# Optimization experiments

Hardware: AMD Instinct MI355X
Metric: run time of the kernel (lower is better)

The kernel has to match this reference:

```python
import jax, jax.numpy as jnp
import numpy as np

H = 128      # hidden_size
B = 8192     # number of sessions
L = 50       # items per session (constant here; code supports ragged)
T = B * L    # total tokens


def setup_inputs() -> dict:
    key = jax.random.key(0)
    ks = jax.random.split(key, 10)
    s = 1.0 / np.sqrt(H)
    u = lambda k, shape: jax.random.uniform(k, shape, jnp.float32, -s, s)
    return {
        "intra_item_emb": jax.random.normal(ks[0], (T, H), jnp.float32),
        "inter_item_emb": jax.random.normal(ks[1], (T, H), jnp.float32),
        "W1": u(ks[2], (H, H)), "b1": u(ks[3], (H,)),
        "W2": u(ks[4], (H, H)), "b2": u(ks[5], (H,)),
        "q_w": u(ks[6], (1, H)), "q_b": u(ks[7], (1,)),
        "W3": u(ks[8], (H, 2 * H)), "b3": u(ks[9], (H,)),
        "seq_len": jnp.full((B,), L, dtype=jnp.int32),
    }


def reference(intra_item_emb, inter_item_emb, W1, b1, W2, b2, q_w, q_b, W3, b3, seq_len):
    # max_fusing: elementwise max of the two embedding streams  [T, H]
    hidden = jnp.maximum(intra_item_emb, inter_item_emb)
    nB = seq_len.shape[0]
    nT = hidden.shape[0]
    # segment id per token and index of last token of each session
    seg_ids = jnp.repeat(jnp.arange(nB), seq_len, total_repeat_length=nT)  # [T]
    last_idx = jnp.cumsum(seq_len) - 1                                      # [B]
    v_n = hidden[last_idx]                 # [B, H] last node of each session
    v_n_rep = v_n[seg_ids]                 # [T, H] broadcast last node to tokens
    # attention weight per token: q(sigmoid(W1 v_n + W2 h))  [T, 1]
    alpha = jax.nn.sigmoid(v_n_rep @ W1.T + b1 + hidden @ W2.T + b2) @ q_w.T + q_b
    # segment-sum pooling of alpha-weighted tokens  [B, H]
    s_g = jax.ops.segment_sum(alpha * hidden, seg_ids, num_segments=nB)
    # final session representation  [B, H]
    h_s = jnp.concatenate([v_n, s_g], axis=1) @ W3.T + b3
    return h_s
```

## Files before the change

### kernel.cpp

```cpp
#include <hip/hip_runtime.h>
#include <hip/hip_bf16.h>

#define HDIM 128
#define RS 136

typedef __attribute__((ext_vector_type(8))) short short8;
typedef __attribute__((ext_vector_type(4))) float floatv4;

static __device__ __forceinline__ unsigned short f2bf(float f) {
  union { float f; unsigned u; } x; x.f = f;
  unsigned r = x.u + 0x7fffu + ((x.u >> 16) & 1u);
  return (unsigned short)(r >> 16);
}
static __device__ __forceinline__ float blo(unsigned u) { return __uint_as_float(u << 16); }
static __device__ __forceinline__ float bhi(unsigned u) { return __uint_as_float(u & 0xffff0000u); }

static __device__ __forceinline__ void sync_lds() {
  asm volatile("s_waitcnt lgkmcnt(0)" ::: "memory");
  __builtin_amdgcn_s_barrier();
  asm volatile("" ::: "memory");
}

__global__ void prep_kernel(const int* __restrict__ seq, int* __restrict__ offs, int B,
                            const float* __restrict__ W1, const float* __restrict__ W2,
                            const float* __restrict__ W3,
                            unsigned short* __restrict__ w1b, unsigned short* __restrict__ w2b,
                            unsigned short* __restrict__ w3b) {
  if (blockIdx.x == 0) {
    __shared__ int part[256];
    int tid = threadIdx.x;
    int chunk = (B + 255) >> 8;
    int beg = tid * chunk, end = min(beg + chunk, B);
    int s = 0;
    for (int i = beg; i < end; ++i) s += seq[i];
    part[tid] = s;
    __syncthreads();
    for (int d = 1; d < 256; d <<= 1) {
      int v = (tid >= d) ? part[tid - d] : 0;
      __syncthreads();
      part[tid] += v;
      __syncthreads();
    }
    int run = (tid == 0) ? 0 : part[tid - 1];
    for (int i = beg; i < end; ++i) { offs[i] = run; run += seq[i]; }
  } else {
    int i = (blockIdx.x - 1) * 256 + threadIdx.x;
    if (i < 16384) { w1b[i] = f2bf(W1[i]); w2b[i] = f2bf(W2[i]); }
    if (i < 32768) { w3b[i] = f2bf(W3[i]); }
  }
}

__global__ __launch_bounds__(256, 3) void session_kernel(
    const float* __restrict__ intra, const float* __restrict__ inter,
    const unsigned short* __restrict__ w1b, const float* __restrict__ b1,
    const unsigned short* __restrict__ w2b, const float* __restrict__ b2,
    const float* __restrict__ qw, const float* __restrict__ qb,
    const unsigned short* __restrict__ w3b, const float* __restrict__ b3,
    const int* __restrict__ seq, const int* __restrict__ offs,
    float* __restrict__ out, int B) {
  __shared__ unsigned short hbf[64 * RS];
  __shared__ unsigned short vnb[HDIM];
  __shared__ unsigned short sgb[HDIM];
  __shared__ float alphaAcc[64];
  __shared__ float sgpart[4][HDIM];

  const int tid = threadIdx.x;
  const int lane = tid & 63, wid = tid >> 6;
  const int quad = lane >> 4, lcol = lane & 15;
  const int nbase = wid << 5;
  const int n0 = nbase + lcol, n1 = n0 + 16;
  const int G = gridDim.x;

  const float qb0 = qb[0];
  const float bb0 = b1[n0] + b2[n0], bb1 = b1[n1] + b2[n1];
  const float q0 = qw[n0], q1 = qw[n1];
  const float b30 = b3[n0], b31 = b3[n1];

  short8 w2f[2][4];
  #pragma unroll
  for (int nt = 0; nt < 2; ++nt) {
    int nn = nbase + (nt << 4) + lcol;
    #pragma unroll
    for (int kt = 0; kt < 4; ++kt)
      w2f[nt][kt] = *(const short8*)(w2b + nn * HDIM + (kt << 5) + (quad << 3));
  }

  float4 ra[8], rb[8];
  int n_cur;
  {
    int s0 = blockIdx.x;
    n_cur = seq[s0]; if (n_cur > 64) n_cur = 64;
    int st0 = offs[s0];
    const float4* pa = (const float4*)(intra + (size_t)st0 * HDIM);
    const float4* pb = (const float4*)(inter + (size_t)st0 * HDIM);
    #pragma unroll
    for (int it = 0; it < 8; ++it) {
      int idx = (it << 8) + tid, t = idx >> 5;
      float4 z; z.x = 0.f; z.y = 0.f; z.z = 0.f; z.w = 0.f;
      float4 va = z, vb = z;
      if (t < n_cur) { va = pa[idx]; vb = pb[idx]; }
      ra[it] = va; rb[it] = vb;
    }
  }

  for (int s = blockIdx.x; s < B; s += G) {
    const int sn = s + G;
    int n_nxt = 0, st_nxt = 0;
    if (sn < B) { n_nxt = seq[sn]; if (n_nxt > 64) n_nxt = 64; st_nxt = offs[sn]; }

    const int lastrow = (n_cur > 0) ? (n_cur - 1) : 0;
    #pragma unroll
    for (int it = 0; it < 8; ++it) {
      int idx = (it << 8) + tid;
      int t = idx >> 5, j4 = idx & 31;
      float4 a = ra[it], c = rb[it];
      union { __hip_bfloat162 b; unsigned u; } p01, p23;
      p01.b = __float22bfloat162_rn(make_float2(fmaxf(a.x, c.x), fmaxf(a.y, c.y)));
      p23.b = __float22bfloat162_rn(make_float2(fmaxf(a.z, c.z), fmaxf(a.w, c.w)));
      uint2 st; st.x = p01.u; st.y = p23.u;
      *(uint2*)&hbf[t * RS + (j4 << 2)] = st;
      if (t == lastrow) *(uint2*)&vnb[j4 << 2] = st;
    }
    if (tid < 64) alphaAcc[tid] = qb0;
    sync_lds();

    float c0, c1;
    {
      floatv4 p0 = {0.f, 0.f, 0.f, 0.f}, p1 = {0.f, 0.f, 0.f, 0.f};
      #pragma unroll
      for (int kt = 0; kt < 4; ++kt) {
        short8 af = *(const short8*)&vnb[(kt << 5) + (quad << 3)];
        short8 bf0 = *(const short8*)(w1b + n0 * HDIM + (kt << 5) + (quad << 3));
        short8 bf1 = *(const short8*)(w1b + n1 * HDIM + (kt << 5) + (quad << 3));
        p0 = __builtin_amdgcn_mfma_f32_16x16x32_bf16(af, bf0, p0, 0, 0, 0);
        p1 = __builtin_amdgcn_mfma_f32_16x16x32_bf16(af, bf1, p1, 0, 0, 0);
      }
      c0 = p0[0] + bb0;
      c1 = p1[0] + bb1;
    }

    if (sn < B) {
      const float4* pa = (const float4*)(intra + (size_t)st_nxt * HDIM);
      const float4* pb = (const float4*)(inter + (size_t)st_nxt * HDIM);
      #pragma unroll
      for (int it = 0; it < 8; ++it) {
        int idx = (it << 8) + tid, t = idx >> 5;
        float4 z; z.x = 0.f; z.y = 0.f; z.z = 0.f; z.w = 0.f;
        float4 va = z, vb = z;
        if (t < n_nxt) { va = pa[idx]; vb = pb[idx]; }
        ra[it] = va; rb[it] = vb;
      }
    }
    asm volatile("" ::: "memory");

    #pragma unroll
    for (int mt = 0; mt < 4; ++mt) {
      floatv4 a0 = {c0, c0, c0, c0}, a1 = {c1, c1, c1, c1};
      const unsigned short* arow = &hbf[((mt << 4) + lcol) * RS + (quad << 3)];
      #pragma unroll
      for (int kt = 0; kt < 4; ++kt) {
        short8 af = *(const short8*)(arow + (kt << 5));
        a0 = __builtin_amdgcn_mfma_f32_16x16x32_bf16(af, w2f[0][kt], a0, 0, 0, 0);
        a1 = __builtin_amdgcn_mfma_f32_16x16x32_bf16(af, w2f[1][kt], a1, 0, 0, 0);
      }
      #pragma unroll
      for (int r = 0; r < 4; ++r) {
        float v = q0 * __builtin_amdgcn_rcpf(1.f + __expf(-a0[r]))
                + q1 * __builtin_amdgcn_rcpf(1.f + __expf(-a1[r]));
        v += __shfl_xor(v, 1, 64);
        v += __shfl_xor(v, 2, 64);
        v += __shfl_xor(v, 4, 64);
        v += __shfl_xor(v, 8, 64);
        if (lcol == 0) atomicAdd(&alphaAcc[(mt << 4) + (quad << 2) + r], v);
      }
    }
    sync_lds();

    {
      int jg = tid & 15, ts = tid >> 4;
      float ac[8];
      #pragma unroll
      for (int e = 0; e < 8; ++e) ac[e] = 0.f;
      #pragma unroll
      for (int tt = 0; tt < 4; ++tt) {
        int t = (tt << 4) + ts;
        float al = alphaAcc[t];
        uint4 u = *(const uint4*)&hbf[t * RS + (jg << 3)];
        ac[0] += al * blo(u.x); ac[1] += al * bhi(u.x);
        ac[2] += al * blo(u.y); ac[3] += al * bhi(u.y);
        ac[4] += al * blo(u.z); ac[5] += al * bhi(u.z);
        ac[6] += al * blo(u.w); ac[7] += al * bhi(u.w);
      }
      #pragma unroll
      for (int e = 0; e < 8; ++e) {
        ac[e] += __shfl_xor(ac[e], 16, 64);
        ac[e] += __shfl_xor(ac[e], 32, 64);
      }
      if (quad == 0) {
        float4 s0v; s0v.x = ac[0]; s0v.y = ac[1]; s0v.z = ac[2]; s0v.w = ac[3];
        float4 s1v; s1v.x = ac[4]; s1v.y = ac[5]; s1v.z = ac[6]; s1v.w = ac[7];
        *(float4*)&sgpart[wid][(jg << 3)] = s0v;
        *(float4*)&sgpart[wid][(jg << 3) + 4] = s1v;
      }
    }
    sync_lds();
    if (tid < HDIM) {
      float sv = sgpart[0][tid] + sgpart[1][tid] + sgpart[2][tid] + sgpart[3][tid];
      sgb[tid] = f2bf(sv);
    }
    sync_lds();

    {
      floatv4 o0 = {0.f, 0.f, 0.f, 0.f}, o1 = {0.f, 0.f, 0.f, 0.f};
      #pragma unroll
      for (int kt = 0; kt < 8; ++kt) {
        const unsigned short* src = (kt < 4) ? &vnb[kt << 5] : &sgb[(kt - 4) << 5];
        short8 af = *(const short8*)(src + (quad << 3));
        short8 bf0 = *(const short8*)(w3b + n0 * 256 + (kt << 5) + (quad << 3));
        short8 bf1 = *(const short8*)(w3b + n1 * 256 + (kt << 5) + (quad << 3));
        o0 = __builtin_amdgcn_mfma_f32_16x16x32_bf16(af, bf0, o0, 0, 0, 0);
        o1 = __builtin_amdgcn_mfma_f32_16x16x32_bf16(af, bf1, o1, 0, 0, 0);
      }
      if (quad == 0) {
        out[(size_t)s * HDIM + n0] = o0[0] + b30;
        out[(size_t)s * HDIM + n1] = o1[0] + b31;
      }
    }
    sync_lds();

    n_cur = n_nxt;
  }
}

extern "C" void kernel_launch(void* const* d_in, const int* in_sizes, int n_in,
                              void* d_out, int out_size, void* d_ws, size_t ws_size,
                              hipStream_t stream) {
  const float* intra = (const float*)d_in[0];
  const float* inter = (const float*)d_in[1];
  const float* W1 = (const float*)d_in[2];
  const float* b1 = (const float*)d_in[3];
  const float* W2 = (const float*)d_in[4];
  const float* b2 = (const float*)d_in[5];
  const float* qw = (const float*)d_in[6];
  const float* qb = (const float*)d_in[7];
  const float* W3 = (const float*)d_in[8];
  const float* b3 = (const float*)d_in[9];
  const int* seq = (const int*)d_in[10];
  const int B = in_sizes[10];
  float* out = (float*)d_out;

  char* ws = (char*)d_ws;
  size_t o1 = (((size_t)B * 4) + 255) & ~(size_t)255;
  int* offs = (int*)ws;
  unsigned short* w1b = (unsigned short*)(ws + o1);
  unsigned short* w2b = (unsigned short*)(ws + o1 + 32768);
  unsigned short* w3b = (unsigned short*)(ws + o1 + 65536);

  int nblk = B < 2048 ? B : 2048;

  hipLaunchKernelGGL(prep_kernel, dim3(129), dim3(256), 0, stream,
                     seq, offs, B, W1, W2, W3, w1b, w2b, w3b);
  hipLaunchKernelGGL(session_kernel, dim3(nblk), dim3(256), 0, stream,
                     intra, inter, w1b, b1, w2b, b2, qw, qb, w3b, b3, seq, offs, out, B);
}
```

Measured before the change: 563.8 us.

## Stream session embeddings into double-buffered LDS via direct global-to-LDS loads

Replaces the register-staged prefetch of the next session with async global_load_lds DMA into two ping-pong LDS buffers, issued right after a full barrier so the copy overlaps the current session's compute. All W1/W2/W3 bf16 fragments are now held in registers for the whole kernel instead of being reloaded per session. The grid drops to 256 persistent blocks at one block per CU, since the raw fp32 buffers use about 128KB of LDS. This lowers register pressure from the prefetch and repeated weight loads, but with one block per CU there is less latency hiding, and the vmcnt(0) barrier each iteration may serialize things.

```diff
diff --git a/kernel.cpp b/kernel.cpp
--- a/kernel.cpp
+++ b/kernel.cpp
@@ -15,10 +15,48 @@
 static __device__ __forceinline__ float blo(unsigned u) { return __uint_as_float(u << 16); }
 static __device__ __forceinline__ float bhi(unsigned u) { return __uint_as_float(u & 0xffff0000u); }
 
+static __device__ __forceinline__ void glds16(const void* g, const void* l) {
+  __builtin_amdgcn_global_load_lds(
+      (const __attribute__((address_space(1))) unsigned int*)(unsigned long long)g,
+      (__attribute__((address_space(3))) unsigned int*)(unsigned long long)l, 16, 0, 0);
+}
+static __device__ __forceinline__ void glds4(const void* g, const void* l) {
+  __builtin_amdgcn_global_load_lds(
+      (const __attribute__((address_space(1))) unsigned int*)(unsigned long long)g,
+      (__attribute__((address_space(3))) unsigned int*)(unsigned long long)l, 4, 0, 0);
+}
+
 static __device__ __forceinline__ void sync_lds() {
   asm volatile("s_waitcnt lgkmcnt(0)" ::: "memory");
   __builtin_amdgcn_s_barrier();
   asm volatile("" ::: "memory");
+}
+static __device__ __forceinline__ void sync_all() {
+  asm volatile("s_waitcnt vmcnt(0) lgkmcnt(0)" ::: "memory");
+  __builtin_amdgcn_s_barrier();
+  asm volatile("" ::: "memory");
+}
+
+static __device__ __forceinline__ void dma_session(
+    const float* __restrict__ intra, const float* __restrict__ inter,
+    int start, int n, float* rawA, float* rawB, int wid, int lane) {
+  const char* ga = (const char*)(intra + (size_t)start * HDIM);
+  const char* gb = (const char*)(inter + (size_t)start * HDIM);
+  char* la = (char*)rawA;
+  char* lb = (char*)rawB;
+  int nfull = n >> 1;
+  for (int i = wid; i < nfull; i += 4) {
+    int off = i << 10;
+    glds16(ga + off + (lane << 4), la + off);
+    glds16(gb + off + (lane << 4), lb + off);
+  }
+  if ((n & 1) && wid == 0) {
+    int off = (n - 1) << 9;
+    glds4(ga + off + (lane << 2), la + off);
+    glds4(ga + off + 256 + (lane << 2), la + off + 256);
+    glds4(gb + off + (lane << 2), lb + off);
+    glds4(gb + off + 256 + (lane << 2), lb + off + 256);
+  }
 }
 
 __global__ void prep_kernel(const int* __restrict__ seq, int* __restrict__ offs, int B,
@@ -50,7 +88,7 @@
   }
 }
 
-__global__ __launch_bounds__(256, 3) void session_kernel(
+__global__ __launch_bounds__(256, 1) void session_kernel(
     const float* __restrict__ intra, const float* __restrict__ inter,
     const unsigned short* __restrict__ w1b, const float* __restrict__ b1,
     const unsigned short* __restrict__ w2b, const float* __restrict__ b2,
@@ -58,6 +96,8 @@
     const unsigned short* __restrict__ w3b, const float* __restrict__ b3,
     const int* __restrict__ seq, const int* __restrict__ offs,
     float* __restrict__ out, int B) {
+  __shared__ float rawA[2][64 * HDIM];
+  __shared__ float rawB[2][64 * HDIM];
   __shared__ unsigned short hbf[64 * RS];
   __shared__ unsigned short vnb[HDIM];
   __shared__ unsigned short sgb[HDIM];
@@ -76,52 +116,65 @@
   const float q0 = qw[n0], q1 = qw[n1];
   const float b30 = b3[n0], b31 = b3[n1];
 
-  short8 w2f[2][4];
+  short8 w1f[2][4], w2f[2][4], w3f[2][8];
   #pragma unroll
-  for (int nt = 0; nt < 2; ++nt) {
-    int nn = nbase + (nt << 4) + lcol;
-    #pragma unroll
-    for (int kt = 0; kt < 4; ++kt)
-      w2f[nt][kt] = *(const short8*)(w2b + nn * HDIM + (kt << 5) + (quad << 3));
-  }
-
-  float4 ra[8], rb[8];
+  for (int kt = 0; kt < 4; ++kt) {
+    w1f[0][kt] = *(const short8*)(w1b + n0 * HDIM + (kt << 5) + (quad << 3));
+    w1f[1][kt] = *(const short8*)(w1b + n1 * HDIM + (kt << 5) + (quad << 3));
+    w2f[0][kt] = *(const short8*)(w2b + n0 * HDIM + (kt << 5) + (quad << 3));
+    w2f[1][kt] = *(const short8*)(w2b + n1 * HDIM + (kt << 5) + (quad << 3));
+  }
+  #pragma unroll
+  for (int kt = 0; kt < 8; ++kt) {
+    w3f[0][kt] = *(const short8*)(w3b + n0 * 256 + (kt << 5) + (quad << 3));
+    w3f[1][kt] = *(const short8*)(w3b + n1 * 256 + (kt << 5) + (quad << 3));
+  }
+
   int n_cur;
   {
     int s0 = blockIdx.x;
     n_cur = seq[s0]; if (n_cur > 64) n_cur = 64;
-    int st0 = offs[s0];
-    const float4* pa = (const float4*)(intra + (size_t)st0 * HDIM);
-    const float4* pb = (const float4*)(inter + (size_t)st0 * HDIM);
-    #pragma unroll
-    for (int it = 0; it < 8; ++it) {
-      int idx = (it << 8) + tid, t = idx >> 5;
-      float4 z; z.x = 0.f; z.y = 0.f; z.z = 0.f; z.w = 0.f;
-      float4 va = z, vb = z;
-      if (t < n_cur) { va = pa[idx]; vb = pb[idx]; }
-      ra[it] = va; rb[it] = vb;
-    }
-  }
+    dma_session(intra, inter, offs[s0], n_cur, rawA[0], rawB[0], wid, lane);
+  }
+  int cur = 0;
 
   for (int s = blockIdx.x; s < B; s += G) {
     const int sn = s + G;
     int n_nxt = 0, st_nxt = 0;
-    if (sn < B) { n_nxt = seq[sn]; if (n_nxt > 64) n_nxt = 64; st_nxt = offs[sn]; }
-
-    const int lastrow = (n_cur > 0) ? (n_cur - 1) : 0;
-    #pragma unroll
-    for (int it = 0; it < 8; ++it) {
-      int idx = (it << 8) + tid;
-      int t = idx >> 5, j4 = idx & 31;
-      float4 a = ra[it], c = rb[it];
-      union { __hip_bfloat162 b; unsigned u; } p01, p23;
-      p01.b = __float22bfloat162_rn(make_float2(fmaxf(a.x, c.x), fmaxf(a.y, c.y)));
-      p23.b = __float22bfloat162_rn(make_float2(fmaxf(a.z, c.z), fmaxf(a.w, c.w)));
-      uint2 st; st.x = p01.u; st.y = p23.u;
-      *(uint2*)&hbf[t * RS + (j4 << 2)] = st;
-      if (t == lastrow) *(uint2*)&vnb[j4 << 2] = st;
-    }
-    if (tid < 64) alphaAcc[tid] = qb0;
+    if (sn < B) {
+      n_nxt = seq[sn]; if (n_nxt > 64) n_nxt = 64;
+      st_nxt = offs[sn];
+    }
+
+    sync_all();
+
+    if (sn < B)
+      dma_session(intra, inter, st_nxt, n_nxt, rawA[cur ^ 1], rawB[cur ^ 1], wid, lane);
+    asm volatile("" ::: "memory");
+
+    {
+      const float4* a4 = (const float4*)rawA[cur];
+      const float4* c4 = (const float4*)rawB[cur];
+      const int lastrow = (n_cur > 0) ? (n_cur - 1) : 0;
+      #pragma unroll
+      for (int it = 0; it < 8; ++it) {
+        int idx = (it << 8) + tid;
+        int t = idx >> 5, j4 = idx & 31;
+        float4 r; r.x = 0.f; r.y = 0.f; r.z = 0.f; r.w = 0.f;
+        if (t < n_cur) {
+          float4 a = a4[idx], c = c4[idx];
+          r.x = fmaxf(a.x, c.x); r.y = fmaxf(a.y, c.y);
+          r.z = fmaxf(a.z, c.z); r.w = fmaxf(a.w, c.w);
+        }
+        union { __hip_bfloat162 b; unsigned u; } p01, p23;
+        p01.b = __float22bfloat162_rn(make_float2(r.x, r.y));
+        p23.b = __float22bfloat162_rn(make_float2(r.z, r.w));
+        uint2 st; st.x = p01.u; st.y = p23.u;
+        *(uint2*)&hbf[t * RS + (j4 << 2)] = st;
+        if (t == lastrow) *(uint2*)&vnb[j4 << 2] = st;
+      }
+      if (tid < 64) alphaAcc[tid] = qb0;
+    }
     sync_lds();
 
     float c0, c1;
@@ -130,28 +183,12 @@
       #pragma unroll
       for (int kt = 0; kt < 4; ++kt) {
         short8 af = *(const short8*)&vnb[(kt << 5) + (quad << 3)];
-        short8 bf0 = *(const short8*)(w1b + n0 * HDIM + (kt << 5) + (quad << 3));
-        short8 bf1 = *(const short8*)(w1b + n1 * HDIM + (kt << 5) + (quad << 3));
-        p0 = __builtin_amdgcn_mfma_f32_16x16x32_bf16(af, bf0, p0, 0, 0, 0);
-        p1 = __builtin_amdgcn_mfma_f32_16x16x32_bf16(af, bf1, p1, 0, 0, 0);
+        p0 = __builtin_amdgcn_mfma_f32_16x16x32_bf16(af, w1f[0][kt], p0, 0, 0, 0);
+        p1 = __builtin_amdgcn_mfma_f32_16x16x32_bf16(af, w1f[1][kt], p1, 0, 0, 0);
       }
       c0 = p0[0] + bb0;
       c1 = p1[0] + bb1;
     }
-
-    if (sn < B) {
-      const float4* pa = (const float4*)(intra + (size_t)st_nxt * HDIM);
-      const float4* pb = (const float4*)(inter + (size_t)st_nxt * HDIM);
-      #pragma unroll
-      for (int it = 0; it < 8; ++it) {
-        int idx = (it << 8) + tid, t = idx >> 5;
-        float4 z; z.x = 0.f; z.y = 0.f; z.z = 0.f; z.w = 0.f;
-        float4 va = z, vb = z;
-        if (t < n_nxt) { va = pa[idx]; vb = pb[idx]; }
-        ra[it] = va; rb[it] = vb;
-      }
-    }
-    asm volatile("" ::: "memory");
 
     #pragma unroll
     for (int mt = 0; mt < 4; ++mt) {
@@ -216,18 +253,16 @@
       for (int kt = 0; kt < 8; ++kt) {
         const unsigned short* src = (kt < 4) ? &vnb[kt << 5] : &sgb[(kt - 4) << 5];
         short8 af = *(const short8*)(src + (quad << 3));
-        short8 bf0 = *(const short8*)(w3b + n0 * 256 + (kt << 5) + (quad << 3));
-        short8 bf1 = *(const short8*)(w3b + n1 * 256 + (kt << 5) + (quad << 3));
-        o0 = __builtin_amdgcn_mfma_f32_16x16x32_bf16(af, bf0, o0, 0, 0, 0);
-        o1 = __builtin_amdgcn_mfma_f32_16x16x32_bf16(af, bf1, o1, 0, 0, 0);
+        o0 = __builtin_amdgcn_mfma_f32_16x16x32_bf16(af, w3f[0][kt], o0, 0, 0, 0);
+        o1 = __builtin_amdgcn_mfma_f32_16x16x32_bf16(af, w3f[1][kt], o1, 0, 0, 0);
       }
       if (quad == 0) {
         out[(size_t)s * HDIM + n0] = o0[0] + b30;
         out[(size_t)s * HDIM + n1] = o1[0] + b31;
       }
     }
-    sync_lds();
-
+
+    cur ^= 1;
     n_cur = n_nxt;
   }
 }
@@ -256,7 +291,7 @@
   unsigned short* w2b = (unsigned short*)(ws + o1 + 32768);
   unsigned short* w3b = (unsigned short*)(ws + o1 + 65536);
 
-  int nblk = B < 2048 ? B : 2048;
+  int nblk = B < 256 ? B : 256;
 
   hipLaunchKernelGGL(prep_kernel, dim3(129), dim3(256), 0, stream,
                      seq, offs, B, W1, W2, W3, w1b, w2b, w3b);
```

Result: faster. 532.6 us (-5.5%).
